# Performance work log

Hardware: AMD Instinct MI355X
Metric: run time of the kernel (lower is better)

The kernel has to match this reference:

```python
import jax, jax.numpy as jnp
import numpy as np

ALPHA = 0.1
K_STEPS = 10


def _with_self_loops(edge_index, n):
    loops = jnp.arange(n, dtype=edge_index.dtype)
    src = jnp.concatenate([edge_index[0], loops])
    dst = jnp.concatenate([edge_index[1], loops])
    return src, dst


def _gcn_norm(src, dst, n, dtype):
    # symmetric normalization deg^{-1/2}[src] * deg^{-1/2}[dst], deg over in-edges (incl. self loops)
    deg = jax.ops.segment_sum(jnp.ones(dst.shape[0], dtype=dtype), dst, num_segments=n)
    dinv = jnp.where(deg > 0, jax.lax.rsqrt(deg), jnp.zeros_like(deg))
    return dinv[src] * dinv[dst]


def _propagate(h, src, dst, norm, n):
    # gather -> scale -> scatter-add (A_hat @ h)
    msg = h[src] * norm[:, None]            # [E, d]
    return jax.ops.segment_sum(msg, dst, num_segments=n)


def setup_inputs() -> dict:
    key = jax.random.key(0)
    ks = jax.random.split(key, 8)
    N, E, D, H, C = 100000, 3200000, 256, 256, 40
    s = 1.0 / np.sqrt(D)
    return {
        "x": jax.random.normal(ks[0], (N, D), dtype=jnp.float32),
        "edge_index": jax.random.randint(ks[1], (2, E), 0, N, dtype=jnp.int64),
        "w1": jax.random.normal(ks[2], (D, H), dtype=jnp.float32) * s,
        "b1": jnp.zeros((H,), dtype=jnp.float32),
        "w2": jax.random.normal(ks[3], (H, H), dtype=jnp.float32) * s,
        "b2": jnp.zeros((H,), dtype=jnp.float32),
        "w3": jax.random.normal(ks[4], (H, H), dtype=jnp.float32) * s,
        "b3": jnp.zeros((H,), dtype=jnp.float32),
        "fc_w": jax.random.normal(ks[5], (H, C), dtype=jnp.float32) * s,
        "fc_b": jnp.zeros((C,), dtype=jnp.float32),
    }


def reference(x, edge_index, w1, b1, w2, b2, w3, b3, fc_w, fc_b):
    n = x.shape[0]
    src, dst = _with_self_loops(edge_index, n)
    norm = _gcn_norm(src, dst, n, x.dtype)

    def gcn_conv(h, w, b):
        h = h @ w                             # linear transform first (PyG GCNConv)
        return _propagate(h, src, dst, norm, n) + b

    h = jax.nn.relu(gcn_conv(x, w1, b1))
    h = jax.nn.relu(gcn_conv(h, w2, b2))
    h = jax.nn.relu(gcn_conv(h, w3, b3))      # convx with layer=3 has one extra GCNConv

    # APPNP: K steps of h <- (1-alpha) * A_hat h + alpha * h0
    h0 = h
    def step(h, _):
        h = (1.0 - ALPHA) * _propagate(h, src, dst, norm, n) + ALPHA * h0
        return h, None
    h, _ = jax.lax.scan(step, h, None, length=K_STEPS)

    logits = h @ fc_w + fc_b
    return jax.nn.log_softmax(logits, axis=1)
```

## Files before the change

### kernel.cpp

```cpp
#include <hip/hip_runtime.h>
#include <math.h>


constexpr int D  = 256;
constexpr int C  = 40;
constexpr int ZP = 64;

typedef _Float16 h2v    __attribute__((ext_vector_type(2)));
typedef _Float16 h4     __attribute__((ext_vector_type(4)));
typedef _Float16 half8v __attribute__((ext_vector_type(8)));
typedef float    f32x4  __attribute__((ext_vector_type(4)));

struct __align__(8) EdgeCV { int c; float v; };


__global__ void k_init_cnt(int* __restrict__ cnt, int N) {
    int i = blockIdx.x * blockDim.x + threadIdx.x;
    if (i < N) cnt[i] = 1;
}

__global__ void k_count(const int* __restrict__ dst, int* __restrict__ cnt, int E) {
    int e = blockIdx.x * blockDim.x + threadIdx.x;
    if (e < E) atomicAdd(&cnt[dst[e]], 1);
}

__global__ void k_alloc(const int* __restrict__ cnt, int* __restrict__ startA,
                        int* __restrict__ cursor, int N) {
    int i = blockIdx.x * blockDim.x + threadIdx.x;
    if (i < N) startA[i] = atomicAdd(cursor, cnt[i]);
}

__global__ void k_selfinit(const int* __restrict__ cnt, const int* __restrict__ startA,
                           float* __restrict__ dinv, EdgeCV* __restrict__ edges,
                           int* __restrict__ fill, int N) {
    int i = blockIdx.x * blockDim.x + threadIdx.x;
    if (i < N) {
        float dv = rsqrtf((float)cnt[i]);
        dinv[i] = dv;
        EdgeCV e; e.c = i; e.v = dv * dv;
        edges[startA[i]] = e;
        fill[i] = 1;
    }
}

__global__ void k_fill_edges(const int* __restrict__ src, const int* __restrict__ dst,
                             const int* __restrict__ startA, const float* __restrict__ dinv,
                             EdgeCV* __restrict__ edges, int* __restrict__ fill, int E) {
    int e = blockIdx.x * blockDim.x + threadIdx.x;
    if (e < E) {
        int s = src[e], d = dst[e];
        int slot = atomicAdd(&fill[d], 1);
        EdgeCV ev; ev.c = s; ev.v = dinv[s] * dinv[d];
        edges[startA[d] + slot] = ev;
    }
}


__global__ void k_transW(const float* __restrict__ W0, const float* __restrict__ W1,
                         const float* __restrict__ W2, _Float16* __restrict__ Wt) {
    int n = blockIdx.x;
    int w = blockIdx.y;
    int k = threadIdx.x;
    const float* W = (w == 0) ? W0 : (w == 1) ? W1 : W2;
    Wt[(size_t)w * 65536 + n * 256 + k] = (_Float16)W[k * 256 + n];
}


template <typename TIN>
__global__ __launch_bounds__(256, 1) void k_gemm_mfma(const TIN* __restrict__ A,
                                                      const _Float16* __restrict__ Wt,
                                                      _Float16* __restrict__ Cout, int M) {
    __shared__ _Float16 wlds[256][72];
    const int tid  = threadIdx.x;
    const int lane = tid & 63;
    const int wave = tid >> 6;
    const int l15  = lane & 15;
    const int lk8  = (lane >> 4) * 8;
    const int rowbase = blockIdx.x * 128 + wave * 32;

    half8v a[2][8];
    #pragma unroll
    for (int mt = 0; mt < 2; ++mt) {
        int row = rowbase + mt * 16 + l15;
        bool ok = row < M;
        const TIN* ap = A + (size_t)(ok ? row : 0) * D;
        #pragma unroll
        for (int kk = 0; kk < 8; ++kk) {
            half8v v;
            if constexpr (sizeof(TIN) == 2) {
                v = *(const half8v*)(ap + kk * 32 + lk8);
            } else {
                float4 f0 = *(const float4*)(ap + kk * 32 + lk8);
                float4 f1 = *(const float4*)(ap + kk * 32 + lk8 + 4);
                v[0] = (_Float16)f0.x; v[1] = (_Float16)f0.y;
                v[2] = (_Float16)f0.z; v[3] = (_Float16)f0.w;
                v[4] = (_Float16)f1.x; v[5] = (_Float16)f1.y;
                v[6] = (_Float16)f1.z; v[7] = (_Float16)f1.w;
            }
            if (!ok) {
                half8v zz = {0, 0, 0, 0, 0, 0, 0, 0};
                v = zz;
            }
            a[mt][kk] = v;
        }
    }

    f32x4 acc[2][16] = {};

    #pragma unroll
    for (int s = 0; s < 4; ++s) {
        {
            const half8v* srcp = (const half8v*)(Wt + (size_t)tid * D + s * 64);
            #pragma unroll
            for (int cc = 0; cc < 8; ++cc)
                *(half8v*)(&wlds[tid][cc * 8]) = srcp[cc];
        }
        __syncthreads();
        #pragma unroll
        for (int kf = 0; kf < 2; ++kf) {
            const int kk = s * 2 + kf;
            #pragma unroll
            for (int nt = 0; nt < 16; ++nt) {
                half8v b = *(const half8v*)(&wlds[nt * 16 + l15][kf * 32 + lk8]);
                acc[0][nt] = __builtin_amdgcn_mfma_f32_16x16x32_f16(a[0][kk], b, acc[0][nt], 0, 0, 0);
                acc[1][nt] = __builtin_amdgcn_mfma_f32_16x16x32_f16(a[1][kk], b, acc[1][nt], 0, 0, 0);
            }
        }
        __syncthreads();
    }

    const int r0 = (lane >> 4) * 4;
    #pragma unroll
    for (int mt = 0; mt < 2; ++mt) {
        #pragma unroll
        for (int r = 0; r < 4; ++r) {
            int row = rowbase + mt * 16 + r0 + r;
            if (row < M) {
                _Float16* crow = Cout + (size_t)row * D;
                #pragma unroll
                for (int nt = 0; nt < 16; ++nt)
                    crow[nt * 16 + l15] = (_Float16)acc[mt][nt][r];
            }
        }
    }
}


__global__ __launch_bounds__(256) void k_spmm_relu(const _Float16* __restrict__ h,
                                                   const int* __restrict__ startA,
                                                   const int* __restrict__ cnt,
                                                   const EdgeCV* __restrict__ edges,
                                                   const float* __restrict__ bias,
                                                   _Float16* __restrict__ out, int N) {
    int gid  = (int)((blockIdx.x * 256u + threadIdx.x) >> 6);
    int lane = threadIdx.x & 63;
    if (gid >= N) return;
    int start = startA[gid], end = start + cnt[gid];
    const h4* hp = (const h4*)h;
    float4 s0 = make_float4(0.f, 0.f, 0.f, 0.f);
    float4 s1 = make_float4(0.f, 0.f, 0.f, 0.f);
    float4 s2 = make_float4(0.f, 0.f, 0.f, 0.f);
    float4 s3 = make_float4(0.f, 0.f, 0.f, 0.f);
    int e = start;
    for (; e + 3 < end; e += 4) {
        EdgeCV c0 = edges[e],     c1 = edges[e + 1];
        EdgeCV c2 = edges[e + 2], c3 = edges[e + 3];
        h4 x0 = hp[(size_t)c0.c * 64 + lane];
        h4 x1 = hp[(size_t)c1.c * 64 + lane];
        h4 x2 = hp[(size_t)c2.c * 64 + lane];
        h4 x3 = hp[(size_t)c3.c * 64 + lane];
        s0.x += c0.v * (float)x0[0]; s0.y += c0.v * (float)x0[1];
        s0.z += c0.v * (float)x0[2]; s0.w += c0.v * (float)x0[3];
        s1.x += c1.v * (float)x1[0]; s1.y += c1.v * (float)x1[1];
        s1.z += c1.v * (float)x1[2]; s1.w += c1.v * (float)x1[3];
        s2.x += c2.v * (float)x2[0]; s2.y += c2.v * (float)x2[1];
        s2.z += c2.v * (float)x2[2]; s2.w += c2.v * (float)x2[3];
        s3.x += c3.v * (float)x3[0]; s3.y += c3.v * (float)x3[1];
        s3.z += c3.v * (float)x3[2]; s3.w += c3.v * (float)x3[3];
    }
    for (; e < end; ++e) {
        EdgeCV c0 = edges[e];
        h4 x0 = hp[(size_t)c0.c * 64 + lane];
        s0.x += c0.v * (float)x0[0]; s0.y += c0.v * (float)x0[1];
        s0.z += c0.v * (float)x0[2]; s0.w += c0.v * (float)x0[3];
    }
    float4 acc = make_float4(s0.x + s1.x + s2.x + s3.x,
                             s0.y + s1.y + s2.y + s3.y,
                             s0.z + s1.z + s2.z + s3.z,
                             s0.w + s1.w + s2.w + s3.w);
    float4 b = ((const float4*)bias)[lane];
    h4 o;
    o[0] = (_Float16)fmaxf(acc.x + b.x, 0.f);
    o[1] = (_Float16)fmaxf(acc.y + b.y, 0.f);
    o[2] = (_Float16)fmaxf(acc.z + b.z, 0.f);
    o[3] = (_Float16)fmaxf(acc.w + b.w, 0.f);
    ((h4*)out)[(size_t)gid * 64 + lane] = o;
}


__global__ __launch_bounds__(256) void k_z0(const _Float16* __restrict__ h,
                                            const float* __restrict__ fcw,
                                            _Float16* __restrict__ z0, int N) {
    __shared__ float ws[D * C];
    for (int i = threadIdx.x; i < D * C; i += 256) ws[i] = fcw[i];
    __syncthreads();
    int row = blockIdx.x * 256 + threadIdx.x;
    if (row >= N) return;
    float acc[C] = {};
    const half8v* hr = (const half8v*)(h + (size_t)row * D);
    for (int kq = 0; kq < 32; ++kq) {
        half8v v = hr[kq];
        #pragma unroll
        for (int j = 0; j < 8; ++j) {
            float hv = (float)v[j];
            #pragma unroll
            for (int c = 0; c < C; ++c) acc[c] += hv * ws[(kq * 8 + j) * C + c];
        }
    }
    h2v* zr = (h2v*)(z0 + (size_t)row * ZP);
    #pragma unroll
    for (int c = 0; c < 20; ++c) {
        h2v o; o[0] = (_Float16)acc[2 * c]; o[1] = (_Float16)acc[2 * c + 1];
        zr[c] = o;
    }
    h2v zz = {(_Float16)0.f, (_Float16)0.f};
    #pragma unroll
    for (int c = 20; c < 32; ++c) zr[c] = zz;
}


__global__ __launch_bounds__(256) void k_spmm40(const _Float16* __restrict__ z,
                                                const int* __restrict__ startA,
                                                const int* __restrict__ cnt,
                                                const EdgeCV* __restrict__ edges,
                                                const _Float16* __restrict__ z0,
                                                _Float16* __restrict__ out, int N) {
    int wid  = (int)((blockIdx.x * 256u + threadIdx.x) >> 6);
    int lane = threadIdx.x & 63;
    int p    = lane >> 5;
    int l5   = lane & 31;
    int row  = wid * 2 + p;
    if (row >= N) return;
    int start = startA[row], end = start + cnt[row];
    const h2v* zp = (const h2v*)z;
    float ax0 = 0.f, ay0 = 0.f, ax1 = 0.f, ay1 = 0.f;
    float ax2 = 0.f, ay2 = 0.f, ax3 = 0.f, ay3 = 0.f;
    int e = start;
    for (; e + 3 < end; e += 4) {
        EdgeCV c0 = edges[e],     c1 = edges[e + 1];
        EdgeCV c2 = edges[e + 2], c3 = edges[e + 3];
        h2v x0 = zp[(size_t)c0.c * 32 + l5];
        h2v x1 = zp[(size_t)c1.c * 32 + l5];
        h2v x2 = zp[(size_t)c2.c * 32 + l5];
        h2v x3 = zp[(size_t)c3.c * 32 + l5];
        ax0 += c0.v * (float)x0[0]; ay0 += c0.v * (float)x0[1];
        ax1 += c1.v * (float)x1[0]; ay1 += c1.v * (float)x1[1];
        ax2 += c2.v * (float)x2[0]; ay2 += c2.v * (float)x2[1];
        ax3 += c3.v * (float)x3[0]; ay3 += c3.v * (float)x3[1];
    }
    for (; e < end; ++e) {
        EdgeCV c0 = edges[e];
        h2v x0 = zp[(size_t)c0.c * 32 + l5];
        ax0 += c0.v * (float)x0[0]; ay0 += c0.v * (float)x0[1];
    }
    float ax = ax0 + ax1 + ax2 + ax3;
    float ay = ay0 + ay1 + ay2 + ay3;
    h2v zz = ((const h2v*)z0)[(size_t)row * 32 + l5];
    ax = 0.9f * ax + 0.1f * (float)zz[0];
    ay = 0.9f * ay + 0.1f * (float)zz[1];
    h2v o; o[0] = (_Float16)ax; o[1] = (_Float16)ay;
    ((h2v*)out)[(size_t)row * 32 + l5] = o;
}


__global__ __launch_bounds__(256) void k_logsm(const _Float16* __restrict__ z,
                                               const float* __restrict__ fcb,
                                               float* __restrict__ out, int N) {
    __shared__ float bs[C];
    for (int i = threadIdx.x; i < C; i += 256) bs[i] = fcb[i];
    __syncthreads();
    int row = blockIdx.x * 256 + threadIdx.x;
    if (row >= N) return;
    float v[C];
    const h2v* zr = (const h2v*)(z + (size_t)row * ZP);
    #pragma unroll
    for (int c = 0; c < 20; ++c) {
        h2v t = zr[c];
        v[2 * c]     = (float)t[0] + bs[2 * c];
        v[2 * c + 1] = (float)t[1] + bs[2 * c + 1];
    }
    float m = v[0];
    #pragma unroll
    for (int c = 1; c < C; ++c) m = fmaxf(m, v[c]);
    float s = 0.f;
    #pragma unroll
    for (int c = 0; c < C; ++c) s += expf(v[c] - m);
    float lse = logf(s) + m;
    float* orow = out + (size_t)row * C;
    #pragma unroll
    for (int c = 0; c < C; ++c) orow[c] = v[c] - lse;
}


extern "C" void kernel_launch(void* const* d_in, const int* in_sizes, int n_in,
                              void* d_out, int out_size, void* d_ws, size_t ws_size,
                              hipStream_t stream) {
    const float* x   = (const float*)d_in[0];
    const int*   ei  = (const int*)d_in[1];
    const float* w1  = (const float*)d_in[2];
    const float* b1  = (const float*)d_in[3];
    const float* w2  = (const float*)d_in[4];
    const float* b2  = (const float*)d_in[5];
    const float* w3  = (const float*)d_in[6];
    const float* b3  = (const float*)d_in[7];
    const float* fcw = (const float*)d_in[8];
    const float* fcb = (const float*)d_in[9];
    float* out = (float*)d_out;

    const int N = in_sizes[0] / D;
    const int E = in_sizes[1] / 2;
    const int* srcArr = ei;
    const int* dstArr = ei + E;

    char* wsp = (char*)d_ws;
    size_t off = 0;
    auto take = [&](size_t bytes) -> void* {
        void* p = wsp + off;
        off = (off + bytes + 255) & ~(size_t)255;
        return p;
    };
    int*       cnt    = (int*)take((size_t)N * 4);
    int*       startA = (int*)take((size_t)N * 4);
    int*       fill   = (int*)take((size_t)N * 4);
    int*       cursor = (int*)take(256);
    float*     dinv   = (float*)take((size_t)N * 4);
    EdgeCV*    edges  = (EdgeCV*)take((size_t)(E + N) * 8);
    _Float16*  bufA   = (_Float16*)take((size_t)N * D * 2);
    _Float16*  bufB   = (_Float16*)take((size_t)N * D * 2);
    _Float16*  bufC   = (_Float16*)take((size_t)N * D * 2);
    _Float16*  Wt     = (_Float16*)take((size_t)3 * D * D * 2);
    _Float16*  z0w    = (_Float16*)take((size_t)N * ZP * 2);
    _Float16*  zA     = (_Float16*)take((size_t)N * ZP * 2);
    _Float16*  zB     = (_Float16*)take((size_t)N * ZP * 2);
    (void)ws_size;

    dim3 b256(256);
    int gN = (N + 255) / 256;
    int gE = (E + 255) / 256;

    hipMemsetAsync(cursor, 0, 4, stream);
    k_init_cnt<<<gN, b256, 0, stream>>>(cnt, N);
    k_count<<<gE, b256, 0, stream>>>(dstArr, cnt, E);
    k_alloc<<<gN, b256, 0, stream>>>(cnt, startA, cursor, N);
    k_selfinit<<<gN, b256, 0, stream>>>(cnt, startA, dinv, edges, fill, N);
    k_fill_edges<<<gE, b256, 0, stream>>>(srcArr, dstArr, startA, dinv, edges, fill, E);

    dim3 tg(256, 3);
    k_transW<<<tg, b256, 0, stream>>>(w1, w2, w3, Wt);

    dim3 gg((N + 127) / 128);
    int spBlocks  = (N + 3) / 4;
    int sp40Blocks = (N + 7) / 8;

    k_gemm_mfma<float><<<gg, b256, 0, stream>>>(x, Wt, bufA, N);
    k_spmm_relu<<<spBlocks, b256, 0, stream>>>(bufA, startA, cnt, edges, b1, bufB, N);
    k_gemm_mfma<_Float16><<<gg, b256, 0, stream>>>(bufB, Wt + 65536, bufA, N);
    k_spmm_relu<<<spBlocks, b256, 0, stream>>>(bufA, startA, cnt, edges, b2, bufB, N);
    k_gemm_mfma<_Float16><<<gg, b256, 0, stream>>>(bufB, Wt + 131072, bufA, N);
    k_spmm_relu<<<spBlocks, b256, 0, stream>>>(bufA, startA, cnt, edges, b3, bufC, N);

    k_z0<<<gN, b256, 0, stream>>>(bufC, fcw, z0w, N);

    const _Float16* zc = z0w;
    _Float16* zn = zA;
    for (int it = 0; it < 10; ++it) {
        k_spmm40<<<sp40Blocks, b256, 0, stream>>>(zc, startA, cnt, edges, z0w, zn, N);
        zc = zn;
        zn = (zn == zA) ? zB : zA;
    }

    k_logsm<<<gN, b256, 0, stream>>>(zc, fcb, out, N);
}
```

Before: 2.093 ms.

## Use nontemporal loads/stores for streamed data and deepen SpMM unroll

Streamed edge lists, GEMM activations, z rows and outputs now go through nontemporal load and store builtins, so gathered feature rows stay in cache longer. The 256-wide SpMM unroll goes from 4 to 8 edges with eight accumulators, putting more gathers in flight. The count-init kernel is replaced by a memset, with the self-loop +1 folded into later uses. Nontemporal hints may hurt if the hardware handles them poorly, and the wider unroll raises register pressure.

```diff
diff --git a/kernel.cpp b/kernel.cpp
--- a/kernel.cpp
+++ b/kernel.cpp
@@ -14,20 +14,47 @@
 struct __align__(8) EdgeCV { int c; float v; };
 
 
-__global__ void k_init_cnt(int* __restrict__ cnt, int N) {
-    int i = blockIdx.x * blockDim.x + threadIdx.x;
-    if (i < N) cnt[i] = 1;
-}
+__device__ inline EdgeCV nt_edge(const EdgeCV* p) {
+    unsigned long long u = __builtin_nontemporal_load((const unsigned long long*)p);
+    EdgeCV e;
+    e.c = (int)(unsigned)(u & 0xffffffffull);
+    e.v = __uint_as_float((unsigned)(u >> 32));
+    return e;
+}
+__device__ inline void nt_store_edge(EdgeCV* p, EdgeCV e) {
+    unsigned long long u = ((unsigned long long)__float_as_uint(e.v) << 32) |
+                           (unsigned long long)(unsigned)e.c;
+    __builtin_nontemporal_store(u, (unsigned long long*)p);
+}
+__device__ inline half8v nt_load_h8(const _Float16* p) {
+    f32x4 f = __builtin_nontemporal_load((const f32x4*)p);
+    return __builtin_bit_cast(half8v, f);
+}
+__device__ inline f32x4 nt_load_f4(const float* p) {
+    return __builtin_nontemporal_load((const f32x4*)p);
+}
+__device__ inline void nt_store_h4(h4* p, h4 v) {
+    __builtin_nontemporal_store(__builtin_bit_cast(unsigned long long, v),
+                                (unsigned long long*)p);
+}
+__device__ inline h2v nt_load_h2(const h2v* p) {
+    unsigned u = __builtin_nontemporal_load((const unsigned*)p);
+    return __builtin_bit_cast(h2v, u);
+}
+
 
 __global__ void k_count(const int* __restrict__ dst, int* __restrict__ cnt, int E) {
     int e = blockIdx.x * blockDim.x + threadIdx.x;
-    if (e < E) atomicAdd(&cnt[dst[e]], 1);
+    if (e < E) {
+        int d = __builtin_nontemporal_load(dst + e);
+        atomicAdd(&cnt[d], 1);
+    }
 }
 
 __global__ void k_alloc(const int* __restrict__ cnt, int* __restrict__ startA,
                         int* __restrict__ cursor, int N) {
     int i = blockIdx.x * blockDim.x + threadIdx.x;
-    if (i < N) startA[i] = atomicAdd(cursor, cnt[i]);
+    if (i < N) startA[i] = atomicAdd(cursor, cnt[i] + 1);
 }
 
 __global__ void k_selfinit(const int* __restrict__ cnt, const int* __restrict__ startA,
@@ -35,10 +62,10 @@
                            int* __restrict__ fill, int N) {
     int i = blockIdx.x * blockDim.x + threadIdx.x;
     if (i < N) {
-        float dv = rsqrtf((float)cnt[i]);
+        float dv = rsqrtf((float)(cnt[i] + 1));
         dinv[i] = dv;
         EdgeCV e; e.c = i; e.v = dv * dv;
-        edges[startA[i]] = e;
+        nt_store_edge(&edges[startA[i]], e);
         fill[i] = 1;
     }
 }
@@ -48,10 +75,11 @@
                              EdgeCV* __restrict__ edges, int* __restrict__ fill, int E) {
     int e = blockIdx.x * blockDim.x + threadIdx.x;
     if (e < E) {
-        int s = src[e], d = dst[e];
+        int s = __builtin_nontemporal_load(src + e);
+        int d = __builtin_nontemporal_load(dst + e);
         int slot = atomicAdd(&fill[d], 1);
         EdgeCV ev; ev.c = s; ev.v = dinv[s] * dinv[d];
-        edges[startA[d] + slot] = ev;
+        nt_store_edge(&edges[startA[d] + slot], ev);
     }
 }
 
@@ -88,14 +116,14 @@
         for (int kk = 0; kk < 8; ++kk) {
             half8v v;
             if constexpr (sizeof(TIN) == 2) {
-                v = *(const half8v*)(ap + kk * 32 + lk8);
+                v = nt_load_h8((const _Float16*)(ap + kk * 32 + lk8));
             } else {
-                float4 f0 = *(const float4*)(ap + kk * 32 + lk8);
-                float4 f1 = *(const float4*)(ap + kk * 32 + lk8 + 4);
-                v[0] = (_Float16)f0.x; v[1] = (_Float16)f0.y;
-                v[2] = (_Float16)f0.z; v[3] = (_Float16)f0.w;
-                v[4] = (_Float16)f1.x; v[5] = (_Float16)f1.y;
-                v[6] = (_Float16)f1.z; v[7] = (_Float16)f1.w;
+                f32x4 f0 = nt_load_f4((const float*)(ap + kk * 32 + lk8));
+                f32x4 f1 = nt_load_f4((const float*)(ap + kk * 32 + lk8 + 4));
+                v[0] = (_Float16)f0[0]; v[1] = (_Float16)f0[1];
+                v[2] = (_Float16)f0[2]; v[3] = (_Float16)f0[3];
+                v[4] = (_Float16)f1[0]; v[5] = (_Float16)f1[1];
+                v[6] = (_Float16)f1[2]; v[7] = (_Float16)f1[3];
             }
             if (!ok) {
                 half8v zz = {0, 0, 0, 0, 0, 0, 0, 0};
@@ -155,46 +183,45 @@
     int gid  = (int)((blockIdx.x * 256u + threadIdx.x) >> 6);
     int lane = threadIdx.x & 63;
     if (gid >= N) return;
-    int start = startA[gid], end = start + cnt[gid];
+    int start = startA[gid], end = start + cnt[gid] + 1;
     const h4* hp = (const h4*)h;
-    float4 s0 = make_float4(0.f, 0.f, 0.f, 0.f);
-    float4 s1 = make_float4(0.f, 0.f, 0.f, 0.f);
-    float4 s2 = make_float4(0.f, 0.f, 0.f, 0.f);
-    float4 s3 = make_float4(0.f, 0.f, 0.f, 0.f);
+    float4 s[8];
+    #pragma unroll
+    for (int i = 0; i < 8; ++i) s[i] = make_float4(0.f, 0.f, 0.f, 0.f);
     int e = start;
-    for (; e + 3 < end; e += 4) {
-        EdgeCV c0 = edges[e],     c1 = edges[e + 1];
-        EdgeCV c2 = edges[e + 2], c3 = edges[e + 3];
+    for (; e + 7 < end; e += 8) {
+        EdgeCV c[8];
+        h4 x[8];
+        #pragma unroll
+        for (int i = 0; i < 8; ++i) c[i] = nt_edge(&edges[e + i]);
+        #pragma unroll
+        for (int i = 0; i < 8; ++i) x[i] = hp[(size_t)c[i].c * 64 + lane];
+        #pragma unroll
+        for (int i = 0; i < 8; ++i) {
+            s[i].x += c[i].v * (float)x[i][0];
+            s[i].y += c[i].v * (float)x[i][1];
+            s[i].z += c[i].v * (float)x[i][2];
+            s[i].w += c[i].v * (float)x[i][3];
+        }
+    }
+    for (; e < end; ++e) {
+        EdgeCV c0 = nt_edge(&edges[e]);
         h4 x0 = hp[(size_t)c0.c * 64 + lane];
-        h4 x1 = hp[(size_t)c1.c * 64 + lane];
-        h4 x2 = hp[(size_t)c2.c * 64 + lane];
-        h4 x3 = hp[(size_t)c3.c * 64 + lane];
-        s0.x += c0.v * (float)x0[0]; s0.y += c0.v * (float)x0[1];
-        s0.z += c0.v * (float)x0[2]; s0.w += c0.v * (float)x0[3];
-        s1.x += c1.v * (float)x1[0]; s1.y += c1.v * (float)x1[1];
-        s1.z += c1.v * (float)x1[2]; s1.w += c1.v * (float)x1[3];
-        s2.x += c2.v * (float)x2[0]; s2.y += c2.v * (float)x2[1];
-        s2.z += c2.v * (float)x2[2]; s2.w += c2.v * (float)x2[3];
-        s3.x += c3.v * (float)x3[0]; s3.y += c3.v * (float)x3[1];
-        s3.z += c3.v * (float)x3[2]; s3.w += c3.v * (float)x3[3];
-    }
-    for (; e < end; ++e) {
-        EdgeCV c0 = edges[e];
-        h4 x0 = hp[(size_t)c0.c * 64 + lane];
-        s0.x += c0.v * (float)x0[0]; s0.y += c0.v * (float)x0[1];
-        s0.z += c0.v * (float)x0[2]; s0.w += c0.v * (float)x0[3];
-    }
-    float4 acc = make_float4(s0.x + s1.x + s2.x + s3.x,
-                             s0.y + s1.y + s2.y + s3.y,
-                             s0.z + s1.z + s2.z + s3.z,
-                             s0.w + s1.w + s2.w + s3.w);
+        s[0].x += c0.v * (float)x0[0]; s[0].y += c0.v * (float)x0[1];
+        s[0].z += c0.v * (float)x0[2]; s[0].w += c0.v * (float)x0[3];
+    }
+    float4 acc = make_float4(0.f, 0.f, 0.f, 0.f);
+    #pragma unroll
+    for (int i = 0; i < 8; ++i) {
+        acc.x += s[i].x; acc.y += s[i].y; acc.z += s[i].z; acc.w += s[i].w;
+    }
     float4 b = ((const float4*)bias)[lane];
     h4 o;
     o[0] = (_Float16)fmaxf(acc.x + b.x, 0.f);
     o[1] = (_Float16)fmaxf(acc.y + b.y, 0.f);
     o[2] = (_Float16)fmaxf(acc.z + b.z, 0.f);
     o[3] = (_Float16)fmaxf(acc.w + b.w, 0.f);
-    ((h4*)out)[(size_t)gid * 64 + lane] = o;
+    nt_store_h4((h4*)out + (size_t)gid * 64 + lane, o);
 }
 
 
@@ -207,9 +234,9 @@
     int row = blockIdx.x * 256 + threadIdx.x;
     if (row >= N) return;
     float acc[C] = {};
-    const half8v* hr = (const half8v*)(h + (size_t)row * D);
+    const _Float16* hr = h + (size_t)row * D;
     for (int kq = 0; kq < 32; ++kq) {
-        half8v v = hr[kq];
+        half8v v = nt_load_h8(hr + kq * 8);
         #pragma unroll
         for (int j = 0; j < 8; ++j) {
             float hv = (float)v[j];
@@ -241,14 +268,16 @@
     int l5   = lane & 31;
     int row  = wid * 2 + p;
     if (row >= N) return;
-    int start = startA[row], end = start + cnt[row];
+    int start = startA[row], end = start + cnt[row] + 1;
     const h2v* zp = (const h2v*)z;
     float ax0 = 0.f, ay0 = 0.f, ax1 = 0.f, ay1 = 0.f;
     float ax2 = 0.f, ay2 = 0.f, ax3 = 0.f, ay3 = 0.f;
     int e = start;
     for (; e + 3 < end; e += 4) {
-        EdgeCV c0 = edges[e],     c1 = edges[e + 1];
-        EdgeCV c2 = edges[e + 2], c3 = edges[e + 3];
+        EdgeCV c0 = nt_edge(&edges[e]);
+        EdgeCV c1 = nt_edge(&edges[e + 1]);
+        EdgeCV c2 = nt_edge(&edges[e + 2]);
+        EdgeCV c3 = nt_edge(&edges[e + 3]);
         h2v x0 = zp[(size_t)c0.c * 32 + l5];
         h2v x1 = zp[(size_t)c1.c * 32 + l5];
         h2v x2 = zp[(size_t)c2.c * 32 + l5];
@@ -259,7 +288,7 @@
         ax3 += c3.v * (float)x3[0]; ay3 += c3.v * (float)x3[1];
     }
     for (; e < end; ++e) {
-        EdgeCV c0 = edges[e];
+        EdgeCV c0 = nt_edge(&edges[e]);
         h2v x0 = zp[(size_t)c0.c * 32 + l5];
         ax0 += c0.v * (float)x0[0]; ay0 += c0.v * (float)x0[1];
     }
@@ -285,7 +314,7 @@
     const h2v* zr = (const h2v*)(z + (size_t)row * ZP);
     #pragma unroll
     for (int c = 0; c < 20; ++c) {
-        h2v t = zr[c];
+        h2v t = nt_load_h2(zr + c);
         v[2 * c]     = (float)t[0] + bs[2 * c];
         v[2 * c + 1] = (float)t[1] + bs[2 * c + 1];
     }
@@ -298,7 +327,8 @@
     float lse = logf(s) + m;
     float* orow = out + (size_t)row * C;
     #pragma unroll
-    for (int c = 0; c < C; ++c) orow[c] = v[c] - lse;
+    for (int c = 0; c < C; ++c)
+        __builtin_nontemporal_store(v[c] - lse, orow + c);
 }
 
 
@@ -349,7 +379,7 @@
     int gE = (E + 255) / 256;
 
     hipMemsetAsync(cursor, 0, 4, stream);
-    k_init_cnt<<<gN, b256, 0, stream>>>(cnt, N);
+    hipMemsetAsync(cnt, 0, (size_t)N * 4, stream);
     k_count<<<gE, b256, 0, stream>>>(dstArr, cnt, E);
     k_alloc<<<gN, b256, 0, stream>>>(cnt, startA, cursor, N);
     k_selfinit<<<gN, b256, 0, stream>>>(cnt, startA, dinv, edges, fill, N);
@@ -359,7 +389,7 @@
     k_transW<<<tg, b256, 0, stream>>>(w1, w2, w3, Wt);
 
     dim3 gg((N + 127) / 128);
-    int spBlocks  = (N + 3) / 4;
+    int spBlocks   = (N + 3) / 4;
     int sp40Blocks = (N + 7) / 8;
 
     k_gemm_mfma<float><<<gg, b256, 0, stream>>>(x, Wt, bufA, N);
```

After: 2.402 ms. +14.8%, slower.
